# Performance work log

Hardware: AMD Instinct MI355X
Metric: run time of the kernel (lower is better)

The kernel has to match this reference:

```python
import jax, jax.numpy as jnp
import numpy as np

B, N, Th, Td, Tw, Tp = 8, 3000, 24, 12, 24, 12
T2a, T2b, K = 64, 32, 3  # hidden temporal dims of the two STBlocks, Cheb order


def _laplacian(A):
    # PyG ChebConv with lambda_max=None -> lambda_max=2.0, sym normalization:
    # L_hat = 2L/lambda_max - I = -D^{-1/2} A D^{-1/2} with zero diagonal
    Aod = A * (1.0 - jnp.eye(A.shape[0], dtype=A.dtype))
    deg = Aod.sum(axis=1)
    dinv = jnp.where(deg > 0, deg ** -0.5, 0.0)
    return -(dinv[:, None] * Aod * dinv[None, :])


def _cheb(x, L, W, b):
    # Chebyshev graph conv, K=3. x: (B,N,Cin), L: (N,N), W: (K,Cin,Cout), b: (Cout,)
    Tx0 = x
    Tx1 = jnp.einsum('nm,bmi->bni', L, Tx0)
    Tx2 = 2.0 * jnp.einsum('nm,bmi->bni', L, Tx1) - Tx0
    out = (jnp.einsum('bni,io->bno', Tx0, W[0])
           + jnp.einsum('bni,io->bno', Tx1, W[1])
           + jnp.einsum('bni,io->bno', Tx2, W[2]))
    return out + b


def _tconv(x, w, b):
    # Conv1d(1, 1, 3, padding=1) over last axis. x: (B,N,T), w: (3,), b: scalar
    xp = jnp.pad(x, ((0, 0), (0, 0), (1, 1)))
    return w[0] * xp[..., :-2] + w[1] * xp[..., 1:-1] + w[2] * xp[..., 2:] + b


def _stblock(x, L, W, bg, cw, cb):
    x = jax.nn.relu(_cheb(x, L, W, bg))
    return jax.nn.relu(_tconv(x, cw, cb))


def _branch(X, L, W1, b1, c1w, c1b, W2, b2, c2w, c2b, WD, bD):
    x = X.reshape(X.shape[0], X.shape[1], X.shape[3])  # (B,N,T)
    x = _stblock(x, L, W1, b1, c1w, c1b)  # (B,N,64)
    x = _stblock(x, L, W2, b2, c2w, c2b)  # (B,N,32)
    return jax.nn.relu(x @ WD + bD)       # (B,N,Tp); forward only uses LinearD


def setup_inputs() -> dict:
    ks = jax.random.split(jax.random.key(0), 48)
    it = iter(range(48))

    def nrm(shape, s=1.0):
        return jax.random.normal(ks[next(it)], shape, jnp.float32) * s

    Xh = nrm((B, N, 1, Th))
    Xd = nrm((B, N, 1, Td))
    Xw = nrm((B, N, 1, Tw))
    u = jax.random.uniform(ks[next(it)], (N, N))
    w = jax.random.uniform(ks[next(it)], (N, N))
    A = jnp.where(u < 0.01, w, 0.0)
    A = 0.5 * (A + A.T)

    def gcn_p(ti, to):
        return nrm((K, ti, to), (2.0 / (ti + to)) ** 0.5), jnp.zeros((to,), jnp.float32)

    def conv_p():
        return nrm((K,), 0.4), nrm((), 0.1)

    Wh1, bh1 = gcn_p(Th, T2a); ch1w, ch1b = conv_p()
    Wh2, bh2 = gcn_p(T2a, T2b); ch2w, ch2b = conv_p()
    Wd1, bd1 = gcn_p(Td, T2a); cd1w, cd1b = conv_p()
    Wd2, bd2 = gcn_p(T2a, T2b); cd2w, cd2b = conv_p()
    Ww1, bw1 = gcn_p(Tw, T2a); cw1w, cw1b = conv_p()
    Ww2, bw2 = gcn_p(T2a, T2b); cw2w, cw2b = conv_p()
    WD = nrm((T2b, Tp), (2.0 / (T2b + Tp)) ** 0.5)
    bD = jnp.zeros((Tp,), jnp.float32)
    Fh = jax.random.uniform(ks[next(it)], (Tp,), jnp.float32)
    Fd = jax.random.uniform(ks[next(it)], (Tp,), jnp.float32)
    Fw = jax.random.uniform(ks[next(it)], (Tp,), jnp.float32)

    return dict(Xh=Xh, Xd=Xd, Xw=Xw, A=A,
                Wh1=Wh1, bh1=bh1, ch1w=ch1w, ch1b=ch1b, Wh2=Wh2, bh2=bh2, ch2w=ch2w, ch2b=ch2b,
                Wd1=Wd1, bd1=bd1, cd1w=cd1w, cd1b=cd1b, Wd2=Wd2, bd2=bd2, cd2w=cd2w, cd2b=cd2b,
                Ww1=Ww1, bw1=bw1, cw1w=cw1w, cw1b=cw1b, Ww2=Ww2, bw2=bw2, cw2w=cw2w, cw2b=cw2b,
                WD=WD, bD=bD, Fh=Fh, Fd=Fd, Fw=Fw)


def reference(Xh, Xd, Xw, A,
              Wh1, bh1, ch1w, ch1b, Wh2, bh2, ch2w, ch2b,
              Wd1, bd1, cd1w, cd1b, Wd2, bd2, cd2w, cd2b,
              Ww1, bw1, cw1w, cw1b, Ww2, bw2, cw2w, cw2b,
              WD, bD, Fh, Fd, Fw):
    L = _laplacian(A)
    Yh = _branch(Xh, L, Wh1, bh1, ch1w, ch1b, Wh2, bh2, ch2w, ch2b, WD, bD)
    Yd = _branch(Xd, L, Wd1, bd1, cd1w, cd1b, Wd2, bd2, cd2w, cd2b, WD, bD)
    Yw = _branch(Xw, L, Ww1, bw1, cw1w, cw1b, Ww2, bw2, cw2w, cw2b, WD, bD)
    Y = Fh * Yh + Fd * Yd + Fw * Yw  # Fusion: elementwise weighted sum over Tp
    return Y[:, :, None, :]  # (B,N,1,Tp)
```

## Files before the change

kernel.cpp:

```cpp
#include <hip/hip_runtime.h>

#define NN 3000
#define NB 8
#define TP 12
#define DMAX 128
#define F1T 480
#define F2T 768

struct BrW {
    const float *W1[3]; const float *b1[3]; const float *c1w[3]; const float *c1b[3];
    const float *W2[3]; const float *b2[3]; const float *c2w[3]; const float *c2b[3];
    const float *Fb[3];
};

__global__ void build_kernel(const float* __restrict__ A, int* __restrict__ colp,
                             float* __restrict__ valp, int* __restrict__ cnt,
                             float* __restrict__ dinv) {
    int n = blockIdx.x;
    int lane = threadIdx.x;
    const float4* row4 = reinterpret_cast<const float4*>(A + (size_t)n * NN);
    int base = 0;
    float s = 0.f;
    for (int start = 0; start < 750; start += 64) {
        int m4 = start + lane;
        float4 v = make_float4(0.f, 0.f, 0.f, 0.f);
        if (m4 < 750) v = row4[m4];
        float vals[4] = {v.x, v.y, v.z, v.w};
        int mbase = m4 * 4;
        #pragma unroll
        for (int u = 0; u < 4; ++u) {
            int m = mbase + u;
            float a = (m4 < 750 && m != n) ? vals[u] : 0.f;
            bool nz = (a != 0.f);
            s += a;
            unsigned long long mask = __ballot(nz);
            int off = __popcll(mask & ((1ull << lane) - 1ull));
            if (nz) {
                int idx = base + off;
                if (idx < DMAX) { colp[n * DMAX + idx] = m; valp[n * DMAX + idx] = a; }
            }
            base += __popcll(mask);
        }
    }
    for (int o = 32; o > 0; o >>= 1) s += __shfl_down(s, o);
    if (lane == 0) {
        cnt[n] = (base < DMAX) ? base : DMAX;
        dinv[n] = (s > 0.f) ? 1.0f / sqrtf(s) : 0.f;
    }
}

__global__ void scale_pack_kernel(const int* __restrict__ colp, float* __restrict__ valp,
                                  const int* __restrict__ cnt, const float* __restrict__ dinv,
                                  const float* __restrict__ Xh, const float* __restrict__ Xd,
                                  const float* __restrict__ Xw, float* __restrict__ xcat) {
    int bid = blockIdx.x;
    if (bid < NN) {
        int n = bid;
        int j = threadIdx.x;
        if (j < DMAX && j < cnt[n]) {
            int m = colp[n * DMAX + j];
            valp[n * DMAX + j] *= -dinv[n] * dinv[m];
        }
    } else {
        int idx = (bid - NN) * 256 + threadIdx.x;
        if (idx >= NN * F1T) return;
        int n = idx / F1T, r = idx % F1T;
        const float* src; int b, t, T;
        if (r < 192)      { src = Xh; T = 24; int rr = r;       b = rr / 24; t = rr % 24; }
        else if (r < 288) { src = Xd; T = 12; int rr = r - 192; b = rr / 12; t = rr % 12; }
        else              { src = Xw; T = 24; int rr = r - 288; b = rr / 24; t = rr % 24; }
        xcat[idx] = src[((size_t)b * NN + n) * T + t];
    }
}

template <int F, int SLICE, int EPI>
__global__ void spmm_kernel(const int* __restrict__ colp, const float* __restrict__ valp,
                            const int* __restrict__ cnt, const float* __restrict__ x,
                            const float* __restrict__ aux, float* __restrict__ y) {
    int nwg = gridDim.x;
    int q = nwg >> 3;
    int bid = blockIdx.x;
    int w = (bid & 7) * q + (bid >> 3);
    int slice = w / NN;
    int n = w - slice * NN;
    int f = slice * SLICE + threadIdx.x;

    __shared__ int   scol[DMAX];
    __shared__ float sval[DMAX];
    int c = cnt[n];
    if (threadIdx.x < DMAX) {
        int j = threadIdx.x;
        bool ok = j < c;
        scol[j] = ok ? colp[n * DMAX + j] * F : 0;
        sval[j] = ok ? valp[n * DMAX + j] : 0.f;
    }
    __syncthreads();
    int c32 = (c + 31) & ~31;
    float a0 = 0.f, a1 = 0.f, a2 = 0.f, a3 = 0.f;
    float a4 = 0.f, a5 = 0.f, a6 = 0.f, a7 = 0.f;
    if (f < F) {
        for (int i = 0; i < c32; i += 32) {
            float g[32], w32[32];
            #pragma unroll
            for (int u = 0; u < 32; ++u) {
                int cc = scol[i + u];
                w32[u] = sval[i + u];
                g[u] = x[cc + f];
            }
            #pragma unroll
            for (int u = 0; u < 32; u += 8) {
                a0 += w32[u + 0] * g[u + 0]; a1 += w32[u + 1] * g[u + 1];
                a2 += w32[u + 2] * g[u + 2]; a3 += w32[u + 3] * g[u + 3];
                a4 += w32[u + 4] * g[u + 4]; a5 += w32[u + 5] * g[u + 5];
                a6 += w32[u + 6] * g[u + 6]; a7 += w32[u + 7] * g[u + 7];
            }
        }
    }
    if (f >= F) return;
    float acc = ((a0 + a1) + (a2 + a3)) + ((a4 + a5) + (a6 + a7));
    size_t o = (size_t)n * F + f;
    if (EPI == 1) acc = 2.f * acc - aux[o];
    else if (EPI == 2) acc = aux[o] + 2.f * acc;
    y[o] = acc;
}

#define SZ_LDA 67
template <int T, int OFF>
__device__ __forceinline__ void fused1_body(
        int tile, int br, const float* __restrict__ xcat, const float* __restrict__ t1cat,
        const float* __restrict__ t2cat, float* __restrict__ y1cat,
        float* __restrict__ y2cat, float* __restrict__ c0cat, const BrW& P, float* smem) {
    constexpr int K = 3 * T;
    constexpr int LDA = K + 1;
    int tid = threadIdx.x;
    float* sW1 = smem;
    float* sX  = smem + K * 64;
    const float* W1 = P.W1[br];
    for (int i = tid; i < K * 64; i += 192) sW1[i] = W1[i];
    int n0 = tile * 12;
    #pragma unroll
    for (int s = 0; s < 3; ++s) {
        const float* src = (s == 0) ? xcat : (s == 1) ? t1cat : t2cat;
        for (int i = tid; i < 96 * T; i += 192) {
            int n_l = i / (8 * T), rem = i % (8 * T);
            int b = rem / T, ii = rem % T;
            sX[(n_l * 8 + b) * LDA + s * T + ii] =
                src[(size_t)(n0 + n_l) * F1T + OFF + b * T + ii];
        }
    }
    __syncthreads();

    int rq = tid >> 3;
    int g  = tid & 7;
    float acc[4][8];
    #pragma unroll
    for (int r = 0; r < 4; ++r)
        #pragma unroll
        for (int j = 0; j < 8; ++j) acc[r][j] = 0.f;

    #pragma unroll 4
    for (int k = 0; k < K; ++k) {
        const float4* wr = reinterpret_cast<const float4*>(sW1 + k * 64 + g * 8);
        float4 wa = wr[0], wb = wr[1];
        #pragma unroll
        for (int r = 0; r < 4; ++r) {
            float zv = sX[(rq * 4 + r) * LDA + k];
            acc[r][0] += zv * wa.x; acc[r][1] += zv * wa.y;
            acc[r][2] += zv * wa.z; acc[r][3] += zv * wa.w;
            acc[r][4] += zv * wb.x; acc[r][5] += zv * wb.y;
            acc[r][6] += zv * wb.z; acc[r][7] += zv * wb.w;
        }
    }

    float bgv[8];
    #pragma unroll
    for (int j = 0; j < 8; ++j) bgv[j] = P.b1[br][g * 8 + j];
    float w0 = P.c1w[br][0], w1 = P.c1w[br][1], w2 = P.c1w[br][2], bb = P.c1b[br][0];

    float o[4][8];
    #pragma unroll
    for (int r = 0; r < 4; ++r) {
        float z[8];
        #pragma unroll
        for (int j = 0; j < 8; ++j) z[j] = fmaxf(acc[r][j] + bgv[j], 0.f);
        float zl = __shfl_up(z[7], 1);
        float zr = __shfl_down(z[0], 1);
        #pragma unroll
        for (int j = 0; j < 8; ++j) {
            float left  = (j > 0) ? z[j - 1] : ((g > 0) ? zl : 0.f);
            float right = (j < 7) ? z[j + 1] : ((g < 7) ? zr : 0.f);
            o[r][j] = fmaxf(w0 * left + w1 * z[j] + w2 * right + bb, 0.f);
        }
    }
    __syncthreads();

    float* sZ  = smem;
    float* sW2 = smem + 96 * SZ_LDA;
    #pragma unroll
    for (int r = 0; r < 4; ++r) {
        float* dst = sZ + (rq * 4 + r) * SZ_LDA + g * 8;
        #pragma unroll
        for (int j = 0; j < 8; ++j) dst[j] = o[r][j];
    }
    const float* W2 = P.W2[br];
    for (int i = tid; i < 6144; i += 192) {
        int k = i / 96, cc = i % 96;
        int j = cc / 3, m = cc % 3;
        sW2[i] = W2[m * 2048 + k * 32 + j];
    }
    __syncthreads();

    float acc2[4][12];
    #pragma unroll
    for (int r = 0; r < 4; ++r)
        #pragma unroll
        for (int j = 0; j < 12; ++j) acc2[r][j] = 0.f;

    #pragma unroll 4
    for (int k = 0; k < 64; ++k) {
        const float4* wr = reinterpret_cast<const float4*>(sW2 + k * 96 + g * 12);
        float4 wa = wr[0], wb = wr[1], wc = wr[2];
        #pragma unroll
        for (int r = 0; r < 4; ++r) {
            float zv = sZ[(rq * 4 + r) * SZ_LDA + k];
            acc2[r][0] += zv * wa.x;  acc2[r][1] += zv * wa.y;
            acc2[r][2] += zv * wa.z;  acc2[r][3] += zv * wa.w;
            acc2[r][4] += zv * wb.x;  acc2[r][5] += zv * wb.y;
            acc2[r][6] += zv * wb.z;  acc2[r][7] += zv * wb.w;
            acc2[r][8] += zv * wc.x;  acc2[r][9] += zv * wc.y;
            acc2[r][10] += zv * wc.z; acc2[r][11] += zv * wc.w;
        }
    }

    const float* b2 = P.b2[br];
    #pragma unroll
    for (int r = 0; r < 4; ++r) {
        int unit = tile * 96 + rq * 4 + r;
        int n = unit >> 3, b = unit & 7;
        size_t obase = (size_t)n * F2T + br * 256 + b * 32;
        #pragma unroll
        for (int jj = 0; jj < 4; ++jj) {
            int j = g * 4 + jj;
            float a0 = acc2[r][jj * 3 + 0], a1 = acc2[r][jj * 3 + 1], a2 = acc2[r][jj * 3 + 2];
            y1cat[obase + j] = a1;
            y2cat[obase + j] = a2;
            c0cat[obase + j] = a0 - a2 + b2[j];
        }
    }
}

__global__ void __launch_bounds__(192, 2)
fused1_kernel(const float* __restrict__ xcat, const float* __restrict__ t1cat,
              const float* __restrict__ t2cat, float* __restrict__ y1cat,
              float* __restrict__ y2cat, float* __restrict__ c0cat, BrW P) {
    __shared__ float smem[12576];
    int b = blockIdx.x;
    if (b < 250)      fused1_body<24, 0>(b, 0, xcat, t1cat, t2cat, y1cat, y2cat, c0cat, P, smem);
    else if (b < 500) fused1_body<12, 192>(b - 250, 1, xcat, t1cat, t2cat, y1cat, y2cat, c0cat, P, smem);
    else              fused1_body<24, 288>(b - 500, 2, xcat, t1cat, t2cat, y1cat, y2cat, c0cat, P, smem);
}

__global__ void combine2_final_kernel(const float* __restrict__ c0cat,
                                      const float* __restrict__ vcat,
                                      const float* __restrict__ WD, const float* __restrict__ bD,
                                      float* __restrict__ out, BrW P) {
    int n = blockIdx.x;
    __shared__ float z2[3][NB][32];
    int unit = threadIdx.x >> 5;
    int co = threadIdx.x & 31;
    int br = unit >> 3, b = unit & 7;
    size_t o = (size_t)n * F2T + br * 256 + b * 32 + co;
    float a = fmaxf(c0cat[o] + vcat[o], 0.f);
    float left  = __shfl_up(a, 1);
    float right = __shfl_down(a, 1);
    if (co == 0) left = 0.f;
    if (co == 31) right = 0.f;
    float w0 = P.c2w[br][0], w1 = P.c2w[br][1], w2 = P.c2w[br][2], bb = P.c2b[br][0];
    z2[br][b][co] = fmaxf(w0 * left + w1 * a + w2 * right + bb, 0.f);
    __syncthreads();
    if (threadIdx.x < NB * TP) {
        int b2 = threadIdx.x / TP, tp = threadIdx.x % TP;
        float y = 0.f;
        for (int brr = 0; brr < 3; ++brr) {
            float s = bD[tp];
            const float* zz = z2[brr][b2];
            for (int c = 0; c < 32; ++c) s += zz[c] * WD[c * TP + tp];
            y += fmaxf(s, 0.f) * P.Fb[brr][tp];
        }
        out[((size_t)b2 * NN + n) * TP + tp] = y;
    }
}


static inline size_t align256(size_t x) { return (x + 255) & ~(size_t)255; }

extern "C" void kernel_launch(void* const* d_in, const int* in_sizes, int n_in,
                              void* d_out, int out_size, void* d_ws, size_t ws_size,
                              hipStream_t stream) {
    const float* Xh = (const float*)d_in[0];
    const float* Xd = (const float*)d_in[1];
    const float* Xw = (const float*)d_in[2];
    const float* A  = (const float*)d_in[3];
    const float* WD = (const float*)d_in[28];
    const float* bD = (const float*)d_in[29];

    BrW P;
    for (int br = 0; br < 3; ++br) {
        int base = 4 + br * 8;
        P.W1[br]  = (const float*)d_in[base + 0];
        P.b1[br]  = (const float*)d_in[base + 1];
        P.c1w[br] = (const float*)d_in[base + 2];
        P.c1b[br] = (const float*)d_in[base + 3];
        P.W2[br]  = (const float*)d_in[base + 4];
        P.b2[br]  = (const float*)d_in[base + 5];
        P.c2w[br] = (const float*)d_in[base + 6];
        P.c2b[br] = (const float*)d_in[base + 7];
        P.Fb[br]  = (const float*)d_in[30 + br];
    }

    char* p = (char*)d_ws;
    int*   colp  = (int*)p;   p += align256((size_t)NN * DMAX * 4);
    float* valp  = (float*)p; p += align256((size_t)NN * DMAX * 4);
    int*   cnt   = (int*)p;   p += align256(NN * 4);
    float* dinv  = (float*)p; p += align256(NN * 4);
    float* xcat  = (float*)p; p += align256((size_t)NN * F1T * 4);
    float* t1cat = (float*)p; p += align256((size_t)NN * F1T * 4);
    float* t2cat = (float*)p; p += align256((size_t)NN * F1T * 4);
    float* y1cat = (float*)p; p += align256((size_t)NN * F2T * 4);
    float* y2cat = (float*)p; p += align256((size_t)NN * F2T * 4);
    float* c0cat = (float*)p; p += align256((size_t)NN * F2T * 4);
    float* scat  = (float*)p; p += align256((size_t)NN * F2T * 4);
    float* vcat  = (float*)p; p += align256((size_t)NN * F2T * 4);

    build_kernel<<<NN, 64, 0, stream>>>(A, colp, valp, cnt, dinv);
    scale_pack_kernel<<<NN + (NN * F1T + 255) / 256, 256, 0, stream>>>(
        colp, valp, cnt, dinv, Xh, Xd, Xw, xcat);

    spmm_kernel<F1T, 256, 0><<<6000, 256, 0, stream>>>(colp, valp, cnt, xcat, nullptr, t1cat);
    spmm_kernel<F1T, 256, 1><<<6000, 256, 0, stream>>>(colp, valp, cnt, t1cat, xcat, t2cat);

    fused1_kernel<<<750, 192, 0, stream>>>(xcat, t1cat, t2cat, y1cat, y2cat, c0cat, P);

    spmm_kernel<F2T, 128, 2><<<18000, 128, 0, stream>>>(colp, valp, cnt, y2cat, y1cat, scat);
    spmm_kernel<F2T, 128, 0><<<18000, 128, 0, stream>>>(colp, valp, cnt, scat, nullptr, vcat);

    combine2_final_kernel<<<NN, 768, 0, stream>>>(c0cat, vcat, WD, bD, (float*)d_out, P);
}
```

Before: 170.1 us.

## Restructure fused dense stage to wave-uniform weight reads with smaller tiles

Rewrites the fused Cheb-weight/temporal-conv/second-weight kernel so each of four waves owns a column slice and each lane owns one (node,batch) row. Weights are read directly from global memory with wave-uniform addresses (scalar loads), so they are no longer staged in LDS. Tiles shrink to 8 nodes, 256 threads per block, and more blocks, which cuts the shared-memory footprint and should raise occupancy. In exchange there are extra barriers and LDS round trips for the temporal-conv neighbours, and each lane does fewer FMAs per LDS load.

```diff
diff --git a/kernel.cpp b/kernel.cpp
--- a/kernel.cpp
+++ b/kernel.cpp
@@ -124,7 +124,6 @@
     y[o] = acc;
 }
 
-#define SZ_LDA 67
 template <int T, int OFF>
 __device__ __forceinline__ void fused1_body(
         int tile, int br, const float* __restrict__ xcat, const float* __restrict__ t1cat,
@@ -133,131 +132,99 @@
     constexpr int K = 3 * T;
     constexpr int LDA = K + 1;
     int tid = threadIdx.x;
-    float* sW1 = smem;
-    float* sX  = smem + K * 64;
-    const float* W1 = P.W1[br];
-    for (int i = tid; i < K * 64; i += 192) sW1[i] = W1[i];
-    int n0 = tile * 12;
+    int lane = tid & 63;
+    int wv = __builtin_amdgcn_readfirstlane(tid >> 6);
+
+    int n0 = tile * 8;
     #pragma unroll
     for (int s = 0; s < 3; ++s) {
         const float* src = (s == 0) ? xcat : (s == 1) ? t1cat : t2cat;
-        for (int i = tid; i < 96 * T; i += 192) {
+        for (int i = tid; i < 64 * T; i += 256) {
             int n_l = i / (8 * T), rem = i % (8 * T);
             int b = rem / T, ii = rem % T;
-            sX[(n_l * 8 + b) * LDA + s * T + ii] =
+            smem[(n_l * 8 + b) * LDA + s * T + ii] =
                 src[(size_t)(n0 + n_l) * F1T + OFF + b * T + ii];
         }
     }
     __syncthreads();
 
-    int rq = tid >> 3;
-    int g  = tid & 7;
-    float acc[4][8];
-    #pragma unroll
-    for (int r = 0; r < 4; ++r)
-        #pragma unroll
-        for (int j = 0; j < 8; ++j) acc[r][j] = 0.f;
-
+    const float* W1p = P.W1[br] + wv * 16;
+    float acc1[16];
+    #pragma unroll
+    for (int j = 0; j < 16; ++j) acc1[j] = 0.f;
     #pragma unroll 4
     for (int k = 0; k < K; ++k) {
-        const float4* wr = reinterpret_cast<const float4*>(sW1 + k * 64 + g * 8);
-        float4 wa = wr[0], wb = wr[1];
+        float zv = smem[lane * LDA + k];
+        const float* wr = W1p + k * 64;
         #pragma unroll
-        for (int r = 0; r < 4; ++r) {
-            float zv = sX[(rq * 4 + r) * LDA + k];
-            acc[r][0] += zv * wa.x; acc[r][1] += zv * wa.y;
-            acc[r][2] += zv * wa.z; acc[r][3] += zv * wa.w;
-            acc[r][4] += zv * wb.x; acc[r][5] += zv * wb.y;
-            acc[r][6] += zv * wb.z; acc[r][7] += zv * wb.w;
-        }
-    }
-
-    float bgv[8];
-    #pragma unroll
-    for (int j = 0; j < 8; ++j) bgv[j] = P.b1[br][g * 8 + j];
+        for (int j = 0; j < 16; ++j) acc1[j] += zv * wr[j];
+    }
+    float z[16];
+    const float* bgp = P.b1[br] + wv * 16;
+    #pragma unroll
+    for (int j = 0; j < 16; ++j) z[j] = fmaxf(acc1[j] + bgp[j], 0.f);
+    __syncthreads();
+
+    #pragma unroll
+    for (int j = 0; j < 16; ++j) smem[lane * 65 + wv * 16 + j] = z[j];
+    __syncthreads();
+
     float w0 = P.c1w[br][0], w1 = P.c1w[br][1], w2 = P.c1w[br][2], bb = P.c1b[br][0];
-
-    float o[4][8];
-    #pragma unroll
-    for (int r = 0; r < 4; ++r) {
-        float z[8];
-        #pragma unroll
-        for (int j = 0; j < 8; ++j) z[j] = fmaxf(acc[r][j] + bgv[j], 0.f);
-        float zl = __shfl_up(z[7], 1);
-        float zr = __shfl_down(z[0], 1);
+    float o[16];
+    #pragma unroll
+    for (int j = 0; j < 16; ++j) {
+        int col = wv * 16 + j;
+        float left  = (j > 0) ? z[j - 1] : ((col > 0) ? smem[lane * 65 + col - 1] : 0.f);
+        float right = (j < 15) ? z[j + 1] : ((col < 63) ? smem[lane * 65 + col + 1] : 0.f);
+        o[j] = fmaxf(w0 * left + w1 * z[j] + w2 * right + bb, 0.f);
+    }
+    __syncthreads();
+
+    #pragma unroll
+    for (int j = 0; j < 16; ++j) smem[lane * 65 + wv * 16 + j] = o[j];
+    __syncthreads();
+
+    const float* W2_0 = P.W2[br] + 0 * 2048 + wv * 8;
+    const float* W2_1 = P.W2[br] + 1 * 2048 + wv * 8;
+    const float* W2_2 = P.W2[br] + 2 * 2048 + wv * 8;
+    float a0[8], a1[8], a2[8];
+    #pragma unroll
+    for (int j = 0; j < 8; ++j) { a0[j] = 0.f; a1[j] = 0.f; a2[j] = 0.f; }
+    #pragma unroll 4
+    for (int k = 0; k < 64; ++k) {
+        float zv = smem[lane * 65 + k];
+        const float* r0 = W2_0 + k * 32;
+        const float* r1 = W2_1 + k * 32;
+        const float* r2 = W2_2 + k * 32;
         #pragma unroll
         for (int j = 0; j < 8; ++j) {
-            float left  = (j > 0) ? z[j - 1] : ((g > 0) ? zl : 0.f);
-            float right = (j < 7) ? z[j + 1] : ((g < 7) ? zr : 0.f);
-            o[r][j] = fmaxf(w0 * left + w1 * z[j] + w2 * right + bb, 0.f);
-        }
-    }
-    __syncthreads();
-
-    float* sZ  = smem;
-    float* sW2 = smem + 96 * SZ_LDA;
-    #pragma unroll
-    for (int r = 0; r < 4; ++r) {
-        float* dst = sZ + (rq * 4 + r) * SZ_LDA + g * 8;
-        #pragma unroll
-        for (int j = 0; j < 8; ++j) dst[j] = o[r][j];
-    }
-    const float* W2 = P.W2[br];
-    for (int i = tid; i < 6144; i += 192) {
-        int k = i / 96, cc = i % 96;
-        int j = cc / 3, m = cc % 3;
-        sW2[i] = W2[m * 2048 + k * 32 + j];
-    }
-    __syncthreads();
-
-    float acc2[4][12];
-    #pragma unroll
-    for (int r = 0; r < 4; ++r)
-        #pragma unroll
-        for (int j = 0; j < 12; ++j) acc2[r][j] = 0.f;
-
-    #pragma unroll 4
-    for (int k = 0; k < 64; ++k) {
-        const float4* wr = reinterpret_cast<const float4*>(sW2 + k * 96 + g * 12);
-        float4 wa = wr[0], wb = wr[1], wc = wr[2];
-        #pragma unroll
-        for (int r = 0; r < 4; ++r) {
-            float zv = sZ[(rq * 4 + r) * SZ_LDA + k];
-            acc2[r][0] += zv * wa.x;  acc2[r][1] += zv * wa.y;
-            acc2[r][2] += zv * wa.z;  acc2[r][3] += zv * wa.w;
-            acc2[r][4] += zv * wb.x;  acc2[r][5] += zv * wb.y;
-            acc2[r][6] += zv * wb.z;  acc2[r][7] += zv * wb.w;
-            acc2[r][8] += zv * wc.x;  acc2[r][9] += zv * wc.y;
-            acc2[r][10] += zv * wc.z; acc2[r][11] += zv * wc.w;
-        }
-    }
-
-    const float* b2 = P.b2[br];
-    #pragma unroll
-    for (int r = 0; r < 4; ++r) {
-        int unit = tile * 96 + rq * 4 + r;
-        int n = unit >> 3, b = unit & 7;
-        size_t obase = (size_t)n * F2T + br * 256 + b * 32;
-        #pragma unroll
-        for (int jj = 0; jj < 4; ++jj) {
-            int j = g * 4 + jj;
-            float a0 = acc2[r][jj * 3 + 0], a1 = acc2[r][jj * 3 + 1], a2 = acc2[r][jj * 3 + 2];
-            y1cat[obase + j] = a1;
-            y2cat[obase + j] = a2;
-            c0cat[obase + j] = a0 - a2 + b2[j];
-        }
-    }
-}
-
-__global__ void __launch_bounds__(192, 2)
+            a0[j] += zv * r0[j];
+            a1[j] += zv * r1[j];
+            a2[j] += zv * r2[j];
+        }
+    }
+
+    int unit = tile * 64 + lane;
+    int n = unit >> 3, b = unit & 7;
+    size_t obase = (size_t)n * F2T + br * 256 + b * 32 + wv * 8;
+    const float* b2p = P.b2[br] + wv * 8;
+    #pragma unroll
+    for (int j = 0; j < 8; ++j) {
+        y1cat[obase + j] = a1[j];
+        y2cat[obase + j] = a2[j];
+        c0cat[obase + j] = a0[j] - a2[j] + b2p[j];
+    }
+}
+
+__global__ void __launch_bounds__(256, 4)
 fused1_kernel(const float* __restrict__ xcat, const float* __restrict__ t1cat,
               const float* __restrict__ t2cat, float* __restrict__ y1cat,
               float* __restrict__ y2cat, float* __restrict__ c0cat, BrW P) {
-    __shared__ float smem[12576];
+    __shared__ float smem[64 * 73];
     int b = blockIdx.x;
-    if (b < 250)      fused1_body<24, 0>(b, 0, xcat, t1cat, t2cat, y1cat, y2cat, c0cat, P, smem);
-    else if (b < 500) fused1_body<12, 192>(b - 250, 1, xcat, t1cat, t2cat, y1cat, y2cat, c0cat, P, smem);
-    else              fused1_body<24, 288>(b - 500, 2, xcat, t1cat, t2cat, y1cat, y2cat, c0cat, P, smem);
+    if (b < 375)      fused1_body<24, 0>(b, 0, xcat, t1cat, t2cat, y1cat, y2cat, c0cat, P, smem);
+    else if (b < 750) fused1_body<12, 192>(b - 375, 1, xcat, t1cat, t2cat, y1cat, y2cat, c0cat, P, smem);
+    else              fused1_body<24, 288>(b - 750, 2, xcat, t1cat, t2cat, y1cat, y2cat, c0cat, P, smem);
 }
 
 __global__ void combine2_final_kernel(const float* __restrict__ c0cat,
@@ -339,7 +306,7 @@
     spmm_kernel<F1T, 256, 0><<<6000, 256, 0, stream>>>(colp, valp, cnt, xcat, nullptr, t1cat);
     spmm_kernel<F1T, 256, 1><<<6000, 256, 0, stream>>>(colp, valp, cnt, t1cat, xcat, t2cat);
 
-    fused1_kernel<<<750, 192, 0, stream>>>(xcat, t1cat, t2cat, y1cat, y2cat, c0cat, P);
+    fused1_kernel<<<1125, 256, 0, stream>>>(xcat, t1cat, t2cat, y1cat, y2cat, c0cat, P);
 
     spmm_kernel<F2T, 128, 2><<<18000, 128, 0, stream>>>(colp, valp, cnt, y2cat, y1cat, scat);
     spmm_kernel<F2T, 128, 0><<<18000, 128, 0, stream>>>(colp, valp, cnt, scat, nullptr, vcat);
```

Result: slower. 198.9 us (+16.9%).
